# Kernel optimization log

Measured on AMD Instinct MI355X. Metric: run time of the kernel, lower is better.

Reference implementation:

```python
import jax, jax.numpy as jnp
import numpy as np

B, L, H, D = 4, 2048, 16, 64

def setup_inputs() -> dict:
    key = jax.random.key(0)
    kq, kk, kv = jax.random.split(key, 3)
    return {
        "queries": jax.random.normal(kq, (B, L, H, D), dtype=jnp.float32),
        "keys": jax.random.normal(kk, (B, L, H, D), dtype=jnp.float32),
        "values": jax.random.normal(kv, (B, L, H, D), dtype=jnp.float32),
    }

def reference(queries, keys, values):
    # [B, L, H, D] -> [B, H, L, D]
    q = jnp.transpose(queries, (0, 2, 1, 3))
    k = jnp.transpose(keys, (0, 2, 1, 3))
    v = jnp.transpose(values, (0, 2, 1, 3))
    d = k.shape[-1]
    scale = 1.0 / jnp.sqrt(jnp.asarray(d, dtype=q.dtype))
    # [B, H, L, L] attention scores
    attn = jnp.einsum("bhqd,bhkd->bhqk", q, k) * scale
    causal = jnp.tril(jnp.ones((q.shape[2], q.shape[2]), dtype=bool))
    attn = jnp.where(causal[None, None, :, :], attn, -jnp.inf)
    p = jax.nn.softmax(attn, axis=-1)  # dropout p=0 -> identity
    y = jnp.einsum("bhqk,bhkd->bhqd", p, v)
    # [B, H, L, D] -> [B, L, H, D]
    return jnp.transpose(y, (0, 2, 1, 3))
```

## Files before the change

kernel.cpp:

```cpp
#include <hip/hip_runtime.h>
#include <hip/hip_bf16.h>

typedef __attribute__((ext_vector_type(8))) short bfrag8;
typedef __attribute__((ext_vector_type(8))) unsigned short u16x8;
typedef __attribute__((ext_vector_type(4))) float f32x4;
typedef __attribute__((ext_vector_type(16))) float f32x16;
typedef __attribute__((ext_vector_type(4))) unsigned int u32x4;

static constexpr int L_ = 2048;
static constexpr int H_ = 16;
static constexpr int D_ = 64;
static constexpr int ROWSTRIDE = H_ * D_;
static constexpr int BSTRIDE = L_ * H_ * D_;
static constexpr size_t NPH = (size_t)L_ * D_;
static constexpr size_t NTOT = (size_t)4 * H_ * L_ * D_;

static constexpr float NEG = -1e30f;
static constexpr float FIXM = 24.0f;
static constexpr float QS = 0.125f * 1.44269504088896341f;

__device__ __forceinline__ unsigned short f2bf(float f) {
  return __builtin_bit_cast(unsigned short, __float2bfloat16(f));
}
__device__ __forceinline__ unsigned int pack2(float lo, float hi) {
  return (unsigned int)f2bf(lo) | ((unsigned int)f2bf(hi) << 16);
}

__device__ __forceinline__ float crosshalf_sum(float x) {
  const unsigned xu = __builtin_bit_cast(unsigned int, x);
  auto r = __builtin_amdgcn_permlane32_swap(xu, xu, false, false);
  return __builtin_bit_cast(float, (unsigned int)r[0]) +
         __builtin_bit_cast(float, (unsigned int)r[1]);
}

__global__ __launch_bounds__(256, 4)
void prep_kernel(const float* __restrict__ K, const float* __restrict__ V,
                 unsigned short* __restrict__ Kb, unsigned short* __restrict__ Vt) {
  const int bid = blockIdx.x;
  const int lt = bid & 31;
  const int bh = bid >> 5;
  const int h = bh & 15;
  const int b = bh >> 4;
  const int l0 = lt * 64;
  const int t = threadIdx.x;
  const int lr = t >> 2;
  const int dc = t & 3;

  __shared__ __align__(16) unsigned short vt[64 * 64];

  const size_t src = ((size_t)(b * L_ + l0 + lr) * H_ + h) * D_ + dc * 16;
  const size_t dst = ((size_t)bh * L_ + l0 + lr) * D_ + dc * 16;

  {
    f32x4 a = *(const f32x4*)(K + src),     b4 = *(const f32x4*)(K + src + 4),
          c4 = *(const f32x4*)(K + src + 8), d4 = *(const f32x4*)(K + src + 12);
    u16x8 o0, o1;
#pragma unroll
    for (int j = 0; j < 4; ++j) {
      o0[j] = f2bf(a[j]);  o0[j + 4] = f2bf(b4[j]);
      o1[j] = f2bf(c4[j]); o1[j + 4] = f2bf(d4[j]);
    }
    *(u16x8*)(Kb + dst) = o0;
    *(u16x8*)(Kb + dst + 8) = o1;
  }
  {
    f32x4 a = *(const f32x4*)(V + src),     b4 = *(const f32x4*)(V + src + 4),
          c4 = *(const f32x4*)(V + src + 8), d4 = *(const f32x4*)(V + src + 12);
    u16x8 o0, o1;
#pragma unroll
    for (int j = 0; j < 4; ++j) {
      o0[j] = f2bf(a[j]);  o0[j + 4] = f2bf(b4[j]);
      o1[j] = f2bf(c4[j]); o1[j + 4] = f2bf(d4[j]);
    }
    const int r7 = (lr + (lr >> 3)) & 7;
    *(u16x8*)&vt[lr * 64 + (((dc * 2) ^ r7) * 8)] = o0;
    *(u16x8*)&vt[lr * 64 + (((dc * 2 + 1) ^ r7) * 8)] = o1;
  }
  __syncthreads();
  {
    const int d = t >> 2;
    const int lc = t & 3;
    const int ch = d >> 3, dl = d & 7;
    u16x8 o0, o1;
#pragma unroll
    for (int i = 0; i < 8; ++i) {
      const int r0 = lc * 16 + i;
      const int r1 = lc * 16 + 8 + i;
      o0[i] = vt[r0 * 64 + ((ch ^ ((r0 + (r0 >> 3)) & 7)) * 8) + dl];
      o1[i] = vt[r1 * 64 + ((ch ^ ((r1 + (r1 >> 3)) & 7)) * 8) + dl];
    }
    const size_t vd = ((size_t)bh * D_ + d) * L_ + l0 + lc * 16;
    *(u16x8*)(Vt + vd) = o0;
    *(u16x8*)(Vt + vd + 8) = o1;
  }
}

__global__ __launch_bounds__(256, 4)
void mha_fwd_db2(const float* __restrict__ Qf,
                 const unsigned short* __restrict__ Kb,
                 const unsigned short* __restrict__ Vt,
                 float* __restrict__ Op) {
  const int bid = blockIdx.x;
  const int plane = bid & 63;
  const int p = 31 - (bid >> 6);
  const int h = plane & 15;
  const int b = plane >> 4;

  const int tid = threadIdx.x;
  const int wv = tid >> 6;
  const int qsel = wv >> 1;
  const int pr = wv & 1;
  const int lane = tid & 63;
  const int q = lane & 31;
  const int hi = lane >> 5;

  const int qt = 2 * p + qsel;
  const int qr0 = qt * 32;
  const int P = p + 1;

  __shared__ __align__(16) unsigned char arena[32768];
  float* mrg = (float*)arena;
  float* lshp = (float*)(arena + 17408);
  float* qstage = (float*)arena;

  const unsigned short* Kh = Kb + (size_t)plane * NPH;
  const unsigned short* Vh = Vt + (size_t)plane * NPH;
  float* Ob = Op + (size_t)b * BSTRIDE + (size_t)h * D_;

  const int kr = tid >> 3, kc = tid & 7;
  const int vr = tid >> 2, vc = tid & 3;
  const int kOff = kr * 64 + ((kc ^ (kr & 7)) * 8);
  const int vOff = vr * 32 + ((vc ^ (vr & 3)) * 8);

  u16x8 k0 = *(const u16x8*)(Kh + (size_t)kr * D_ + kc * 8);
  u16x8 v0 = *(const u16x8*)(Vh + (size_t)vr * L_ + vc * 8);
  u16x8 k1 = *(const u16x8*)(Kh + (size_t)(32 + kr) * D_ + kc * 8);
  u16x8 v1 = *(const u16x8*)(Vh + (size_t)vr * L_ + 32 + vc * 8);

  {
    const float* qbase = Qf + ((size_t)(b * L_ + 64 * p)) * ROWSTRIDE + h * D_;
#pragma unroll
    for (int i = 0; i < 4; ++i) {
      const int c4 = tid + 256 * i;
      const int row = c4 >> 4;
      const int cin = c4 & 15;
      const f32x4 v = *(const f32x4*)(qbase + (size_t)row * ROWSTRIDE + cin * 4);
      *(f32x4*)&qstage[row * 68 + cin * 4] = v;
    }
  }
  __syncthreads();

  bfrag8 qB[4];
#pragma unroll
  for (int s = 0; s < 4; ++s) {
    const float* qrow = &qstage[(qsel * 32 + q) * 68 + 16 * s + 8 * hi];
    const f32x4 lo = *(const f32x4*)qrow;
    const f32x4 hi4 = *(const f32x4*)(qrow + 4);
    bfrag8 f;
#pragma unroll
    for (int j = 0; j < 4; ++j) {
      f[j]     = (short)f2bf(lo[j] * QS);
      f[j + 4] = (short)f2bf(hi4[j] * QS);
    }
    qB[s] = f;
  }
  __syncthreads();

  {
    *(u16x8*)((unsigned short*)(arena) + kOff) = k0;
    *(u16x8*)((unsigned short*)(arena + 4096) + kOff) = k1;
    *(u16x8*)((unsigned short*)(arena + 16384) + vOff) = v0;
    *(u16x8*)((unsigned short*)(arena + 16384 + 4096) + vOff) = v1;
  }
  __syncthreads();

  float lp = 0.f;
  f32x16 o0 = {};
  f32x16 o1 = {};

  for (int k = 0; k < P; ++k) {
    const int cur = k & 1;
    const int t = 2 * k + pr;
    const bool more = (k + 1 < P);
    const bool docomp = (t <= qt);

    u16x8 kn0, vn0, kn1, vn1;
    if (more) {
      const int base = (k + 1) * 64;
      kn0 = *(const u16x8*)(Kh + (size_t)(base + kr) * D_ + kc * 8);
      vn0 = *(const u16x8*)(Vh + (size_t)vr * L_ + base + vc * 8);
      kn1 = *(const u16x8*)(Kh + (size_t)(base + 32 + kr) * D_ + kc * 8);
      vn1 = *(const u16x8*)(Vh + (size_t)vr * L_ + base + 32 + vc * 8);
    }

    f32x16 sacc = {};
    if (docomp) {
      const unsigned short* kb =
          (const unsigned short*)(arena + (size_t)(cur * 2 + pr) * 4096);
      bfrag8 kA[4];
#pragma unroll
      for (int s = 0; s < 4; ++s)
        kA[s] = *(const bfrag8*)&kb[q * 64 + (((2 * s + hi) ^ (q & 7)) * 8)];
      __builtin_amdgcn_s_setprio(1);
#pragma unroll
      for (int s = 0; s < 4; ++s)
        sacc = __builtin_amdgcn_mfma_f32_32x32x16_bf16(kA[s], qB[s], sacc, 0, 0, 0);
      __builtin_amdgcn_s_setprio(0);
    }

    if (more) {
      unsigned char* kslab = arena + (size_t)((cur ^ 1) * 2) * 4096;
      unsigned char* vslab = arena + 16384 + (size_t)((cur ^ 1) * 2) * 4096;
      *(u16x8*)((unsigned short*)kslab + kOff) = kn0;
      *(u16x8*)((unsigned short*)(kslab + 4096) + kOff) = kn1;
      *(u16x8*)((unsigned short*)vslab + vOff) = vn0;
      *(u16x8*)((unsigned short*)(vslab + 4096) + vOff) = vn1;
    }

    if (docomp) {
      if (t == qt) {
#pragma unroll
        for (int r = 0; r < 16; ++r) {
          const int crow = (r & 3) + 8 * (r >> 2) + 4 * hi;
          if (crow > q) sacc[r] = NEG;
        }
      }

#pragma unroll
      for (int r = 0; r < 16; ++r) sacc[r] = __builtin_exp2f(sacc[r] - FIXM);
      {
        float s8[8];
#pragma unroll
        for (int r = 0; r < 8; ++r) s8[r] = sacc[2 * r] + sacc[2 * r + 1];
#pragma unroll
        for (int r = 0; r < 4; ++r) s8[r] += s8[r + 4];
        lp += (s8[0] + s8[2]) + (s8[1] + s8[3]);
      }

      const unsigned int a0 = pack2(sacc[0],  sacc[1]),  a1 = pack2(sacc[2],  sacc[3]);
      const unsigned int a2 = pack2(sacc[4],  sacc[5]),  a3 = pack2(sacc[6],  sacc[7]);
      const unsigned int a4 = pack2(sacc[8],  sacc[9]),  a5 = pack2(sacc[10], sacc[11]);
      const unsigned int a6 = pack2(sacc[12], sacc[13]), a7 = pack2(sacc[14], sacc[15]);
      auto r02 = __builtin_amdgcn_permlane32_swap(a0, a2, false, false);
      auto r13 = __builtin_amdgcn_permlane32_swap(a1, a3, false, false);
      auto r46 = __builtin_amdgcn_permlane32_swap(a4, a6, false, false);
      auto r57 = __builtin_amdgcn_permlane32_swap(a5, a7, false, false);
      u32x4 w0, w1;
      w0[0] = r02[0]; w0[1] = r13[0]; w0[2] = r02[1]; w0[3] = r13[1];
      w1[0] = r46[0]; w1[1] = r57[0]; w1[2] = r46[1]; w1[3] = r57[1];
      const bfrag8 pb0 = __builtin_bit_cast(bfrag8, w0);
      const bfrag8 pb1 = __builtin_bit_cast(bfrag8, w1);

      const unsigned short* vb =
          (const unsigned short*)(arena + 16384 + (size_t)(cur * 2 + pr) * 4096);
      bfrag8 vA[2][2];
#pragma unroll
      for (int ks = 0; ks < 2; ++ks)
#pragma unroll
        for (int dh = 0; dh < 2; ++dh)
          vA[ks][dh] = *(const bfrag8*)&vb[(32 * dh + q) * 32 + (((2 * ks + hi) ^ (q & 3)) * 8)];

      __builtin_amdgcn_s_setprio(1);
      o0 = __builtin_amdgcn_mfma_f32_32x32x16_bf16(vA[0][0], pb0, o0, 0, 0, 0);
      o0 = __builtin_amdgcn_mfma_f32_32x32x16_bf16(vA[1][0], pb1, o0, 0, 0, 0);
      o1 = __builtin_amdgcn_mfma_f32_32x32x16_bf16(vA[0][1], pb0, o1, 0, 0, 0);
      o1 = __builtin_amdgcn_mfma_f32_32x32x16_bf16(vA[1][1], pb1, o1, 0, 0, 0);
      __builtin_amdgcn_s_setprio(0);
    }

    __syncthreads();
  }

  const float lfull = crosshalf_sum(lp);
  float* mrow = mrg + (qsel * 32 + q) * 68;
  if (pr == 1) {
#pragma unroll
    for (int r2 = 0; r2 < 4; ++r2) {
      f32x4 s0, s1;
#pragma unroll
      for (int j = 0; j < 4; ++j) { s0[j] = o0[4 * r2 + j]; s1[j] = o1[4 * r2 + j]; }
      *(f32x4*)&mrow[8 * r2 + 4 * hi] = s0;
      *(f32x4*)&mrow[32 + 8 * r2 + 4 * hi] = s1;
    }
    if (hi == 0) lshp[qsel * 32 + q] = lfull;
  }
  __syncthreads();
  if (pr == 0) {
    const float inv = 1.f / (lfull + lshp[qsel * 32 + q]);
    float* orow = Ob + (size_t)(qr0 + q) * ROWSTRIDE;
#pragma unroll
    for (int r2 = 0; r2 < 4; ++r2) {
      const f32x4 pB0 = *(const f32x4*)&mrow[8 * r2 + 4 * hi];
      const f32x4 pB1 = *(const f32x4*)&mrow[32 + 8 * r2 + 4 * hi];
      f32x4 s0, s1;
#pragma unroll
      for (int j = 0; j < 4; ++j) {
        s0[j] = (o0[4 * r2 + j] + pB0[j]) * inv;
        s1[j] = (o1[4 * r2 + j] + pB1[j]) * inv;
      }
      *(f32x4*)(orow + 8 * r2 + 4 * hi) = s0;
      *(f32x4*)(orow + 32 + 8 * r2 + 4 * hi) = s1;
    }
  }
}

__global__ __launch_bounds__(256, 4)
void mha_fwd_f32(const float* __restrict__ Qp, const float* __restrict__ Kp,
                 const float* __restrict__ Vp, float* __restrict__ Op) {
  const int bid = blockIdx.x;
  const int qt = 31 - (bid & 31);
  const int bh = bid >> 5;
  const int h = bh & 15;
  const int b = bh >> 4;
  const int tid = threadIdx.x;
  const int w = tid >> 6;
  const int lane = tid & 63;
  const int g = lane >> 4;
  const int c = lane & 15;

  __shared__ __align__(16) unsigned short Pb[4][16 * 64];
  unsigned short* P = Pb[w];

  const size_t base = (size_t)b * BSTRIDE + (size_t)h * D_;
  const float* Qb = Qp + base;
  const float* Kb = Kp + base;
  const float* Vb = Vp + base;
  float* Ob = Op + base;
  const int qr0 = qt * 64 + w * 16;

  bfrag8 qf[2];
  {
    const float* qp = Qb + (size_t)(qr0 + c) * ROWSTRIDE + g * 8;
#pragma unroll
    for (int s = 0; s < 2; ++s) {
      f32x4 a0 = *(const f32x4*)(qp + 32 * s);
      f32x4 a1 = *(const f32x4*)(qp + 32 * s + 4);
      bfrag8 f;
#pragma unroll
      for (int j = 0; j < 4; ++j) {
        f[j] = (short)f2bf(a0[j] * 0.125f);
        f[j + 4] = (short)f2bf(a1[j] * 0.125f);
      }
      qf[s] = f;
    }
  }
  float m_i[4], l_i[4];
  f32x4 oacc[4];
#pragma unroll
  for (int i = 0; i < 4; ++i) {
    m_i[i] = -INFINITY; l_i[i] = 0.f;
    oacc[i][0] = oacc[i][1] = oacc[i][2] = oacc[i][3] = 0.f;
  }
  for (int t = 0; t <= qt; ++t) {
    const int kv0 = t * 64;
    const bool diag = (t == qt);
    const int kbmax = diag ? w : 3;
    f32x4 sacc[4];
#pragma unroll
    for (int kb = 0; kb < 4; ++kb) {
      if (kb <= kbmax) {
        f32x4 acc; acc[0] = acc[1] = acc[2] = acc[3] = 0.f;
        const float* kp = Kb + (size_t)(kv0 + kb * 16 + c) * ROWSTRIDE + g * 8;
#pragma unroll
        for (int s = 0; s < 2; ++s) {
          f32x4 a0 = *(const f32x4*)(kp + 32 * s);
          f32x4 a1 = *(const f32x4*)(kp + 32 * s + 4);
          bfrag8 kf;
#pragma unroll
          for (int j = 0; j < 4; ++j) {
            kf[j] = (short)f2bf(a0[j]);
            kf[j + 4] = (short)f2bf(a1[j]);
          }
          acc = __builtin_amdgcn_mfma_f32_16x16x32_bf16(qf[s], kf, acc, 0, 0, 0);
        }
        if (diag && kb == w) {
#pragma unroll
          for (int i = 0; i < 4; ++i)
            if (c > 4 * g + i) acc[i] = -INFINITY;
        }
        sacc[kb] = acc;
      } else {
        sacc[kb][0] = sacc[kb][1] = sacc[kb][2] = sacc[kb][3] = -INFINITY;
      }
    }
    float tmax[4];
#pragma unroll
    for (int i = 0; i < 4; ++i)
      tmax[i] = fmaxf(fmaxf(sacc[0][i], sacc[1][i]), fmaxf(sacc[2][i], sacc[3][i]));
#pragma unroll
    for (int mk = 1; mk <= 8; mk <<= 1)
#pragma unroll
      for (int i = 0; i < 4; ++i) tmax[i] = fmaxf(tmax[i], __shfl_xor(tmax[i], mk));
    float rsum[4];
#pragma unroll
    for (int i = 0; i < 4; ++i) {
      const float mnew = fmaxf(m_i[i], tmax[i]);
      const float sc = __expf(m_i[i] - mnew);
      m_i[i] = mnew;
      float rs = 0.f;
#pragma unroll
      for (int kb = 0; kb < 4; ++kb) {
        const float p = __expf(sacc[kb][i] - mnew);
        sacc[kb][i] = p; rs += p;
      }
      rsum[i] = rs; l_i[i] *= sc;
#pragma unroll
      for (int db = 0; db < 4; ++db) oacc[db][i] *= sc;
    }
#pragma unroll
    for (int mk = 1; mk <= 8; mk <<= 1)
#pragma unroll
      for (int i = 0; i < 4; ++i) rsum[i] += __shfl_xor(rsum[i], mk);
#pragma unroll
    for (int i = 0; i < 4; ++i) l_i[i] += rsum[i];
#pragma unroll
    for (int kb = 0; kb < 4; ++kb) {
      const int col = kb * 16 + c;
      const int chunk = col >> 3;
      const int lo = col & 7;
#pragma unroll
      for (int i = 0; i < 4; ++i) {
        const int row = 4 * g + i;
        P[row * 64 + ((chunk ^ (row & 7)) * 8) + lo] = f2bf(sacc[kb][i]);
      }
    }
    asm volatile("s_waitcnt lgkmcnt(0)" ::: "memory");
    bfrag8 pa[2];
#pragma unroll
    for (int ks = 0; ks < 2; ++ks) {
      const int row = c;
      const int chunk = (4 * ks + g) ^ (row & 7);
      pa[ks] = *(const bfrag8*)&P[row * 64 + chunk * 8];
    }
#pragma unroll
    for (int ks = 0; ks < 2; ++ks) {
      const float* vp = Vb + (size_t)(kv0 + ks * 32 + g * 8) * ROWSTRIDE + c;
#pragma unroll
      for (int db = 0; db < 4; ++db) {
        bfrag8 vf;
#pragma unroll
        for (int j = 0; j < 8; ++j)
          vf[j] = (short)f2bf(vp[(size_t)j * ROWSTRIDE + db * 16]);
        oacc[db] = __builtin_amdgcn_mfma_f32_16x16x32_bf16(pa[ks], vf, oacc[db], 0, 0, 0);
      }
    }
  }
#pragma unroll
  for (int i = 0; i < 4; ++i) {
    const float inv = 1.f / l_i[i];
    const int qq = qr0 + 4 * g + i;
    float* op = Ob + (size_t)qq * ROWSTRIDE + c;
#pragma unroll
    for (int db = 0; db < 4; ++db)
      op[db * 16] = oacc[db][i] * inv;
  }
}

extern "C" void kernel_launch(void* const* d_in, const int* in_sizes, int n_in,
                              void* d_out, int out_size, void* d_ws, size_t ws_size,
                              hipStream_t stream) {
  const float* Q = (const float*)d_in[0];
  const float* K = (const float*)d_in[1];
  const float* V = (const float*)d_in[2];
  float* O = (float*)d_out;

  const size_t need = 2 * NTOT * sizeof(unsigned short);
  if (ws_size >= need) {
    unsigned short* Kb = (unsigned short*)d_ws;
    unsigned short* Vt = Kb + NTOT;
    prep_kernel<<<dim3(2048), dim3(256), 0, stream>>>(K, V, Kb, Vt);
    mha_fwd_db2<<<dim3(2048), dim3(256), 0, stream>>>(Q, Kb, Vt, O);
  } else {
    mha_fwd_f32<<<dim3(2048), dim3(256), 0, stream>>>(Q, K, V, O);
  }
}
```

Measured before the change: 87.81 us.

## Give each wave a full 32-row query tile over both key halves, 128 rows per block

The attention kernel now assigns each of the four waves its own 32-row query tile (128 query rows per block, 1024 blocks). Each wave processes both 32-key halves of every 64-key tile, instead of two waves splitting the keys and merging partial outputs through shared memory. This removes the end-of-kernel LDS merge and its extra barrier, and halves the number of K/V tile loads per query row. In exchange, per-wave work and register pressure double (launch bounds drop to 2), there are fewer blocks to balance the causal workload, and the Q staging uses an XOR swizzle instead of padding to fit 128 rows.

```diff
diff --git a/kernel.cpp b/kernel.cpp
--- a/kernel.cpp
+++ b/kernel.cpp
@@ -95,32 +95,28 @@
   }
 }
 
-__global__ __launch_bounds__(256, 4)
-void mha_fwd_db2(const float* __restrict__ Qf,
+__global__ __launch_bounds__(256, 2)
+void mha_fwd_c64(const float* __restrict__ Qf,
                  const unsigned short* __restrict__ Kb,
                  const unsigned short* __restrict__ Vt,
                  float* __restrict__ Op) {
   const int bid = blockIdx.x;
   const int plane = bid & 63;
-  const int p = 31 - (bid >> 6);
+  const int g = 15 - (bid >> 6);
   const int h = plane & 15;
   const int b = plane >> 4;
 
   const int tid = threadIdx.x;
   const int wv = tid >> 6;
-  const int qsel = wv >> 1;
-  const int pr = wv & 1;
   const int lane = tid & 63;
   const int q = lane & 31;
   const int hi = lane >> 5;
 
-  const int qt = 2 * p + qsel;
+  const int qt = 4 * g + wv;
   const int qr0 = qt * 32;
-  const int P = p + 1;
+  const int P = 2 * g + 2;
 
   __shared__ __align__(16) unsigned char arena[32768];
-  float* mrg = (float*)arena;
-  float* lshp = (float*)(arena + 17408);
   float* qstage = (float*)arena;
 
   const unsigned short* Kh = Kb + (size_t)plane * NPH;
@@ -138,14 +134,14 @@
   u16x8 v1 = *(const u16x8*)(Vh + (size_t)vr * L_ + 32 + vc * 8);
 
   {
-    const float* qbase = Qf + ((size_t)(b * L_ + 64 * p)) * ROWSTRIDE + h * D_;
-#pragma unroll
-    for (int i = 0; i < 4; ++i) {
+    const float* qbase = Qf + ((size_t)(b * L_ + 128 * g)) * ROWSTRIDE + h * D_;
+#pragma unroll
+    for (int i = 0; i < 8; ++i) {
       const int c4 = tid + 256 * i;
       const int row = c4 >> 4;
       const int cin = c4 & 15;
       const f32x4 v = *(const f32x4*)(qbase + (size_t)row * ROWSTRIDE + cin * 4);
-      *(f32x4*)&qstage[row * 68 + cin * 4] = v;
+      *(f32x4*)&qstage[row * 64 + ((cin ^ (row & 15)) * 4)] = v;
     }
   }
   __syncthreads();
@@ -153,9 +149,10 @@
   bfrag8 qB[4];
 #pragma unroll
   for (int s = 0; s < 4; ++s) {
-    const float* qrow = &qstage[(qsel * 32 + q) * 68 + 16 * s + 8 * hi];
-    const f32x4 lo = *(const f32x4*)qrow;
-    const f32x4 hi4 = *(const f32x4*)(qrow + 4);
+    const int row = 32 * wv + q;
+    const int c0 = 4 * s + 2 * hi;
+    const f32x4 lo = *(const f32x4*)&qstage[row * 64 + ((c0 ^ (row & 15)) * 4)];
+    const f32x4 hi4 = *(const f32x4*)&qstage[row * 64 + (((c0 + 1) ^ (row & 15)) * 4)];
     bfrag8 f;
 #pragma unroll
     for (int j = 0; j < 4; ++j) {
@@ -166,12 +163,10 @@
   }
   __syncthreads();
 
-  {
-    *(u16x8*)((unsigned short*)(arena) + kOff) = k0;
-    *(u16x8*)((unsigned short*)(arena + 4096) + kOff) = k1;
-    *(u16x8*)((unsigned short*)(arena + 16384) + vOff) = v0;
-    *(u16x8*)((unsigned short*)(arena + 16384 + 4096) + vOff) = v1;
-  }
+  *(u16x8*)((unsigned short*)(arena) + kOff) = k0;
+  *(u16x8*)((unsigned short*)(arena + 4096) + kOff) = k1;
+  *(u16x8*)((unsigned short*)(arena + 16384) + vOff) = v0;
+  *(u16x8*)((unsigned short*)(arena + 16384 + 4096) + vOff) = v1;
   __syncthreads();
 
   float lp = 0.f;
@@ -180,9 +175,11 @@
 
   for (int k = 0; k < P; ++k) {
     const int cur = k & 1;
-    const int t = 2 * k + pr;
+    const int t0 = 2 * k;
+    const int t1 = 2 * k + 1;
     const bool more = (k + 1 < P);
-    const bool docomp = (t <= qt);
+    const bool do0 = (t0 <= qt);
+    const bool do1 = (t1 <= qt);
 
     u16x8 kn0, vn0, kn1, vn1;
     if (more) {
@@ -193,18 +190,31 @@
       vn1 = *(const u16x8*)(Vh + (size_t)vr * L_ + base + 32 + vc * 8);
     }
 
-    f32x16 sacc = {};
-    if (docomp) {
-      const unsigned short* kb =
-          (const unsigned short*)(arena + (size_t)(cur * 2 + pr) * 4096);
+    f32x16 sa = {}, sb = {};
+    if (do0) {
+      const unsigned short* kbp =
+          (const unsigned short*)(arena + (size_t)(cur * 2) * 4096);
       bfrag8 kA[4];
 #pragma unroll
       for (int s = 0; s < 4; ++s)
-        kA[s] = *(const bfrag8*)&kb[q * 64 + (((2 * s + hi) ^ (q & 7)) * 8)];
+        kA[s] = *(const bfrag8*)&kbp[q * 64 + (((2 * s + hi) ^ (q & 7)) * 8)];
       __builtin_amdgcn_s_setprio(1);
 #pragma unroll
       for (int s = 0; s < 4; ++s)
-        sacc = __builtin_amdgcn_mfma_f32_32x32x16_bf16(kA[s], qB[s], sacc, 0, 0, 0);
+        sa = __builtin_amdgcn_mfma_f32_32x32x16_bf16(kA[s], qB[s], sa, 0, 0, 0);
+      __builtin_amdgcn_s_setprio(0);
+    }
+    if (do1) {
+      const unsigned short* kbp =
+          (const unsigned short*)(arena + (size_t)(cur * 2 + 1) * 4096);
+      bfrag8 kA[4];
+#pragma unroll
+      for (int s = 0; s < 4; ++s)
+        kA[s] = *(const bfrag8*)&kbp[q * 64 + (((2 * s + hi) ^ (q & 7)) * 8)];
+      __builtin_amdgcn_s_setprio(1);
+#pragma unroll
+      for (int s = 0; s < 4; ++s)
+        sb = __builtin_amdgcn_mfma_f32_32x32x16_bf16(kA[s], qB[s], sb, 0, 0, 0);
       __builtin_amdgcn_s_setprio(0);
     }
 
@@ -217,30 +227,28 @@
       *(u16x8*)((unsigned short*)(vslab + 4096) + vOff) = vn1;
     }
 
-    if (docomp) {
-      if (t == qt) {
+    if (do0) {
+      if (t0 == qt) {
 #pragma unroll
         for (int r = 0; r < 16; ++r) {
           const int crow = (r & 3) + 8 * (r >> 2) + 4 * hi;
-          if (crow > q) sacc[r] = NEG;
+          if (crow > q) sa[r] = NEG;
         }
       }
-
-#pragma unroll
-      for (int r = 0; r < 16; ++r) sacc[r] = __builtin_exp2f(sacc[r] - FIXM);
+#pragma unroll
+      for (int r = 0; r < 16; ++r) sa[r] = __builtin_exp2f(sa[r] - FIXM);
       {
         float s8[8];
 #pragma unroll
-        for (int r = 0; r < 8; ++r) s8[r] = sacc[2 * r] + sacc[2 * r + 1];
+        for (int r = 0; r < 8; ++r) s8[r] = sa[2 * r] + sa[2 * r + 1];
 #pragma unroll
         for (int r = 0; r < 4; ++r) s8[r] += s8[r + 4];
         lp += (s8[0] + s8[2]) + (s8[1] + s8[3]);
       }
-
-      const unsigned int a0 = pack2(sacc[0],  sacc[1]),  a1 = pack2(sacc[2],  sacc[3]);
-      const unsigned int a2 = pack2(sacc[4],  sacc[5]),  a3 = pack2(sacc[6],  sacc[7]);
-      const unsigned int a4 = pack2(sacc[8],  sacc[9]),  a5 = pack2(sacc[10], sacc[11]);
-      const unsigned int a6 = pack2(sacc[12], sacc[13]), a7 = pack2(sacc[14], sacc[15]);
+      const unsigned int a0 = pack2(sa[0],  sa[1]),  a1 = pack2(sa[2],  sa[3]);
+      const unsigned int a2 = pack2(sa[4],  sa[5]),  a3 = pack2(sa[6],  sa[7]);
+      const unsigned int a4 = pack2(sa[8],  sa[9]),  a5 = pack2(sa[10], sa[11]);
+      const unsigned int a6 = pack2(sa[12], sa[13]), a7 = pack2(sa[14], sa[15]);
       auto r02 = __builtin_amdgcn_permlane32_swap(a0, a2, false, false);
       auto r13 = __builtin_amdgcn_permlane32_swap(a1, a3, false, false);
       auto r46 = __builtin_amdgcn_permlane32_swap(a4, a6, false, false);
@@ -250,16 +258,14 @@
       w1[0] = r46[0]; w1[1] = r57[0]; w1[2] = r46[1]; w1[3] = r57[1];
       const bfrag8 pb0 = __builtin_bit_cast(bfrag8, w0);
       const bfrag8 pb1 = __builtin_bit_cast(bfrag8, w1);
-
       const unsigned short* vb =
-          (const unsigned short*)(arena + 16384 + (size_t)(cur * 2 + pr) * 4096);
+          (const unsigned short*)(arena + 16384 + (size_t)(cur * 2) * 4096);
       bfrag8 vA[2][2];
 #pragma unroll
       for (int ks = 0; ks < 2; ++ks)
 #pragma unroll
         for (int dh = 0; dh < 2; ++dh)
           vA[ks][dh] = *(const bfrag8*)&vb[(32 * dh + q) * 32 + (((2 * ks + hi) ^ (q & 3)) * 8)];
-
       __builtin_amdgcn_s_setprio(1);
       o0 = __builtin_amdgcn_mfma_f32_32x32x16_bf16(vA[0][0], pb0, o0, 0, 0, 0);
       o0 = __builtin_amdgcn_mfma_f32_32x32x16_bf16(vA[1][0], pb1, o0, 0, 0, 0);
@@ -267,40 +273,70 @@
       o1 = __builtin_amdgcn_mfma_f32_32x32x16_bf16(vA[1][1], pb1, o1, 0, 0, 0);
       __builtin_amdgcn_s_setprio(0);
     }
+    if (do1) {
+      if (t1 == qt) {
+#pragma unroll
+        for (int r = 0; r < 16; ++r) {
+          const int crow = (r & 3) + 8 * (r >> 2) + 4 * hi;
+          if (crow > q) sb[r] = NEG;
+        }
+      }
+#pragma unroll
+      for (int r = 0; r < 16; ++r) sb[r] = __builtin_exp2f(sb[r] - FIXM);
+      {
+        float s8[8];
+#pragma unroll
+        for (int r = 0; r < 8; ++r) s8[r] = sb[2 * r] + sb[2 * r + 1];
+#pragma unroll
+        for (int r = 0; r < 4; ++r) s8[r] += s8[r + 4];
+        lp += (s8[0] + s8[2]) + (s8[1] + s8[3]);
+      }
+      const unsigned int a0 = pack2(sb[0],  sb[1]),  a1 = pack2(sb[2],  sb[3]);
+      const unsigned int a2 = pack2(sb[4],  sb[5]),  a3 = pack2(sb[6],  sb[7]);
+      const unsigned int a4 = pack2(sb[8],  sb[9]),  a5 = pack2(sb[10], sb[11]);
+      const unsigned int a6 = pack2(sb[12], sb[13]), a7 = pack2(sb[14], sb[15]);
+      auto r02 = __builtin_amdgcn_permlane32_swap(a0, a2, false, false);
+      auto r13 = __builtin_amdgcn_permlane32_swap(a1, a3, false, false);
+      auto r46 = __builtin_amdgcn_permlane32_swap(a4, a6, false, false);
+      auto r57 = __builtin_amdgcn_permlane32_swap(a5, a7, false, false);
+      u32x4 w0, w1;
+      w0[0] = r02[0]; w0[1] = r13[0]; w0[2] = r02[1]; w0[3] = r13[1];
+      w1[0] = r46[0]; w1[1] = r57[0]; w1[2] = r46[1]; w1[3] = r57[1];
+      const bfrag8 pb0 = __builtin_bit_cast(bfrag8, w0);
+      const bfrag8 pb1 = __builtin_bit_cast(bfrag8, w1);
+      const unsigned short* vb =
+          (const unsigned short*)(arena + 16384 + (size_t)(cur * 2 + 1) * 4096);
+      bfrag8 vA[2][2];
+#pragma unroll
+      for (int ks = 0; ks < 2; ++ks)
+#pragma unroll
+        for (int dh = 0; dh < 2; ++dh)
+          vA[ks][dh] = *(const bfrag8*)&vb[(32 * dh + q) * 32 + (((2 * ks + hi) ^ (q & 3)) * 8)];
+      __builtin_amdgcn_s_setprio(1);
+      o0 = __builtin_amdgcn_mfma_f32_32x32x16_bf16(vA[0][0], pb0, o0, 0, 0, 0);
+      o0 = __builtin_amdgcn_mfma_f32_32x32x16_bf16(vA[1][0], pb1, o0, 0, 0, 0);
+      o1 = __builtin_amdgcn_mfma_f32_32x32x16_bf16(vA[0][1], pb0, o1, 0, 0, 0);
+      o1 = __builtin_amdgcn_mfma_f32_32x32x16_bf16(vA[1][1], pb1, o1, 0, 0, 0);
+      __builtin_amdgcn_s_setprio(0);
+    }
 
     __syncthreads();
   }
 
   const float lfull = crosshalf_sum(lp);
-  float* mrow = mrg + (qsel * 32 + q) * 68;
-  if (pr == 1) {
-#pragma unroll
-    for (int r2 = 0; r2 < 4; ++r2) {
-      f32x4 s0, s1;
-#pragma unroll
-      for (int j = 0; j < 4; ++j) { s0[j] = o0[4 * r2 + j]; s1[j] = o1[4 * r2 + j]; }
-      *(f32x4*)&mrow[8 * r2 + 4 * hi] = s0;
-      *(f32x4*)&mrow[32 + 8 * r2 + 4 * hi] = s1;
-    }
-    if (hi == 0) lshp[qsel * 32 + q] = lfull;
-  }
-  __syncthreads();
-  if (pr == 0) {
-    const float inv = 1.f / (lfull + lshp[qsel * 32 + q]);
-    float* orow = Ob + (size_t)(qr0 + q) * ROWSTRIDE;
-#pragma unroll
-    for (int r2 = 0; r2 < 4; ++r2) {
-      const f32x4 pB0 = *(const f32x4*)&mrow[8 * r2 + 4 * hi];
-      const f32x4 pB1 = *(const f32x4*)&mrow[32 + 8 * r2 + 4 * hi];
-      f32x4 s0, s1;
-#pragma unroll
-      for (int j = 0; j < 4; ++j) {
-        s0[j] = (o0[4 * r2 + j] + pB0[j]) * inv;
-        s1[j] = (o1[4 * r2 + j] + pB1[j]) * inv;
-      }
-      *(f32x4*)(orow + 8 * r2 + 4 * hi) = s0;
-      *(f32x4*)(orow + 32 + 8 * r2 + 4 * hi) = s1;
-    }
+  const float inv = 1.f / lfull;
+
+  float* orow = Ob + (size_t)(qr0 + q) * ROWSTRIDE;
+#pragma unroll
+  for (int r2 = 0; r2 < 4; ++r2) {
+    f32x4 s0, s1;
+#pragma unroll
+    for (int j = 0; j < 4; ++j) {
+      s0[j] = o0[4 * r2 + j] * inv;
+      s1[j] = o1[4 * r2 + j] * inv;
+    }
+    *(f32x4*)(orow + 8 * r2 + 4 * hi) = s0;
+    *(f32x4*)(orow + 32 + 8 * r2 + 4 * hi) = s1;
   }
 }
 
@@ -469,7 +505,7 @@
     unsigned short* Kb = (unsigned short*)d_ws;
     unsigned short* Vt = Kb + NTOT;
     prep_kernel<<<dim3(2048), dim3(256), 0, stream>>>(K, V, Kb, Vt);
-    mha_fwd_db2<<<dim3(2048), dim3(256), 0, stream>>>(Q, Kb, Vt, O);
+    mha_fwd_c64<<<dim3(1024), dim3(256), 0, stream>>>(Q, Kb, Vt, O);
   } else {
     mha_fwd_f32<<<dim3(2048), dim3(256), 0, stream>>>(Q, K, V, O);
   }
```

After: 91.16 us. 3.8% more time.
